# Optimization experiments

Measured on AMD Instinct MI355X. Metric: run time of the kernel, lower is better.

The kernel has to match this reference:

```python
import jax, jax.numpy as jnp
import numpy as np

TEMPERATURE = 0.5
EPS = 1e-12  # matches torch F.normalize default eps


def _l2_normalize(x):
    norm = jnp.sqrt(jnp.sum(x * x, axis=1, keepdims=True))
    return x / jnp.maximum(norm, EPS)


def setup_inputs() -> dict:
    key = jax.random.key(0)
    k1, k2 = jax.random.split(key)
    proj_1 = jax.random.normal(k1, (4096, 128), dtype=jnp.float32)
    proj_2 = jax.random.normal(k2, (4096, 128), dtype=jnp.float32)
    return {"proj_1": proj_1, "proj_2": proj_2}


def reference(proj_1, proj_2):
    batch_size = proj_1.shape[0]
    z_i = _l2_normalize(proj_1)
    z_j = _l2_normalize(proj_2)
    reps = jnp.concatenate([z_i, z_j], axis=0)  # [2B, D], rows unit-norm
    # cosine similarity of unit-norm rows == dot product -> single matmul
    sim = reps @ reps.T  # [2B, 2B]
    # positives: diag offset +B and -B
    pos_ij = jnp.diagonal(sim, offset=batch_size)   # [B]
    pos_ji = jnp.diagonal(sim, offset=-batch_size)  # [B]
    positives = jnp.concatenate([pos_ij, pos_ji], axis=0)  # [2B]
    nominator = jnp.exp(positives / TEMPERATURE)
    n = 2 * batch_size
    mask = 1.0 - jnp.eye(n, dtype=sim.dtype)
    denominator = jnp.sum(mask * jnp.exp(sim / TEMPERATURE), axis=1)  # [2B]
    all_losses = -jnp.log(nominator / denominator)
    return jnp.sum(all_losses) / n
```

## Files before the change

kernel.cpp:

```cpp
#include <hip/hip_runtime.h>
#include <stdint.h>


#define TEMP 0.5f
#define EXP2_SCALE 2.885390081777927f

typedef __bf16 bf16_t;
typedef bf16_t bf16x8 __attribute__((ext_vector_type(8)));
typedef float floatx4 __attribute__((ext_vector_type(4)));

typedef __attribute__((address_space(3))) uint32_t lds_u32;
typedef const __attribute__((address_space(1))) uint32_t glb_u32;

__device__ __forceinline__ unsigned short f32_to_bf16(float f) {
    union { float f; uint32_t u; } v; v.f = f;
    uint32_t u = v.u;
    uint32_t r = (u + 0x7FFFu + ((u >> 16) & 1u)) >> 16;
    return (unsigned short)r;
}

__device__ __forceinline__ bf16x8 as_bf16x8(uint4 v) {
    union { uint4 u; bf16x8 b; } c; c.u = v; return c.b;
}

__global__ __launch_bounds__(256) void norm_pos_kernel(
        const float* __restrict__ p1, const float* __restrict__ p2,
        unsigned short* __restrict__ reps, float* __restrict__ pos,
        float* __restrict__ rowsum, int B) {
    if (threadIdx.x < 8) {
        int z = blockIdx.x * 8 + threadIdx.x;
        if (z < 2 * B) rowsum[z] = 0.f;
    }

    int wave = threadIdx.x >> 6;
    int lane = threadIdx.x & 63;
    int i = blockIdx.x * 4 + wave;
    if (i >= B) return;

    const float2* r1 = (const float2*)(p1 + (size_t)i * 128);
    const float2* r2 = (const float2*)(p2 + (size_t)i * 128);
    float2 a = r1[lane];
    float2 b = r2[lane];
    float ss1 = a.x * a.x + a.y * a.y;
    float ss2 = b.x * b.x + b.y * b.y;
    float d   = a.x * b.x + a.y * b.y;
    #pragma unroll
    for (int off = 32; off > 0; off >>= 1) {
        ss1 += __shfl_xor(ss1, off);
        ss2 += __shfl_xor(ss2, off);
        d   += __shfl_xor(d,   off);
    }
    float rn1 = rsqrtf(fmaxf(ss1, 1e-24f));
    float rn2 = rsqrtf(fmaxf(ss2, 1e-24f));

    ushort2* z1 = (ushort2*)reps + (size_t)i * 64;
    ushort2* z2 = (ushort2*)reps + (size_t)(B + i) * 64;
    z1[lane] = make_ushort2(f32_to_bf16(a.x * rn1), f32_to_bf16(a.y * rn1));
    z2[lane] = make_ushort2(f32_to_bf16(b.x * rn2), f32_to_bf16(b.y * rn2));

    if (lane == 0) pos[i] = d * rn1 * rn2;
}

__global__ __launch_bounds__(256) void simexp_kernel(
        const unsigned short* __restrict__ reps,
        float* __restrict__ rowsum, int nt) {
    const int tid  = threadIdx.x;
    const int wave = tid >> 6;
    const int lane = tid & 63;
    const int quad = lane >> 4;
    const int l16  = lane & 15;

    int rem = (int)blockIdx.x;
    int by = 0;
    while (rem >= nt - by) { rem -= nt - by; ++by; }
    const int bx = by + rem;
    const bool diag = (bx == by);

    const int rowWave = by * 128 + wave * 32;
    const int colBase = bx * 128;

    const uint4* g = (const uint4*)reps;

    __shared__ __align__(16) unsigned short bbuf[2][2048];
    __shared__ float lds_cs[4][128];

    lds_cs[wave][lane]      = 0.f;
    lds_cs[wave][lane + 64] = 0.f;

    bf16x8 a[2][4];
    #pragma unroll
    for (int t = 0; t < 2; ++t)
        #pragma unroll
        for (int ks = 0; ks < 4; ++ks)
            a[t][ks] = as_bf16x8(g[(size_t)(rowWave + t * 16 + l16) * 16 + ks * 4 + quad]);

    float rs[2][4];
    #pragma unroll
    for (int t = 0; t < 2; ++t)
        #pragma unroll
        for (int r = 0; r < 4; ++r) rs[t][r] = 0.f;

    const int s_ks  = tid >> 6;
    const int s_fl  = tid & 63;
    const int s_fq  = s_fl >> 4;
    const int s_f16 = s_fl & 15;
    auto stage = [&](int buf, int ct) {
        const unsigned short* src = reps
            + (size_t)(colBase + ct * 16 + s_f16) * 128 + s_ks * 32 + s_fq * 8;
        __builtin_amdgcn_global_load_lds(
            (glb_u32*)src, (lds_u32*)&bbuf[buf][tid * 8], 16, 0, 0);
    };

    stage(0, 0);
    int cur = 0;

    #pragma unroll 1
    for (int ct = 0; ct < 8; ++ct) {
        __syncthreads();
        if (ct < 7) stage(cur ^ 1, ct + 1);

        bf16x8 b[4];
        #pragma unroll
        for (int ks = 0; ks < 4; ++ks)
            b[ks] = *(const bf16x8*)&bbuf[cur][ks * 512 + lane * 8];

        floatx4 acc[2];
        #pragma unroll
        for (int t = 0; t < 2; ++t) acc[t] = (floatx4){0.f, 0.f, 0.f, 0.f};
        #pragma unroll
        for (int ks = 0; ks < 4; ++ks)
            #pragma unroll
            for (int t = 0; t < 2; ++t)
                acc[t] = __builtin_amdgcn_mfma_f32_16x16x32_bf16(a[t][ks], b[ks], acc[t], 0, 0, 0);

        const int c = colBase + ct * 16 + l16;
        if (!diag) {
            float cs = 0.f;
            #pragma unroll
            for (int t = 0; t < 2; ++t)
                #pragma unroll
                for (int r = 0; r < 4; ++r) {
                    float e = exp2f(acc[t][r] * EXP2_SCALE);
                    rs[t][r] += e;
                    cs += e;
                }
            cs += __shfl_xor(cs, 16);
            cs += __shfl_xor(cs, 32);
            if (lane < 16) lds_cs[wave][ct * 16 + lane] += cs;
        } else {
            #pragma unroll
            for (int t = 0; t < 2; ++t) {
                const int rb = rowWave + t * 16 + quad * 4;
                #pragma unroll
                for (int r = 0; r < 4; ++r) {
                    float e = (rb + r == c) ? 0.f : exp2f(acc[t][r] * EXP2_SCALE);
                    rs[t][r] += e;
                }
            }
        }
        cur ^= 1;
    }

    #pragma unroll
    for (int off = 1; off < 16; off <<= 1)
        #pragma unroll
        for (int t = 0; t < 2; ++t)
            #pragma unroll
            for (int r = 0; r < 4; ++r)
                rs[t][r] += __shfl_xor(rs[t][r], off);

    if (l16 == 0) {
        #pragma unroll
        for (int t = 0; t < 2; ++t)
            #pragma unroll
            for (int r = 0; r < 4; ++r)
                atomicAdd(&rowsum[rowWave + t * 16 + quad * 4 + r], rs[t][r]);
    }

    if (!diag) {
        __syncthreads();
        if (tid < 128)
            atomicAdd(&rowsum[colBase + tid],
                      lds_cs[0][tid] + lds_cs[1][tid] + lds_cs[2][tid] + lds_cs[3][tid]);
    }
}

__global__ __launch_bounds__(1024) void finalize_kernel(
        const float* __restrict__ rowsum, const float* __restrict__ pos,
        float* __restrict__ out, int N2, int B) {
    float v = 0.f;
    const float4* r4 = (const float4*)rowsum;
    const int n4 = N2 >> 2;
    for (int k = threadIdx.x; k < n4; k += 1024) {
        float4 x = r4[k];
        v += logf(x.x) + logf(x.y) + logf(x.z) + logf(x.w);
    }
    float p = 0.f;
    const float4* p4 = (const float4*)pos;
    const int b4 = B >> 2;
    for (int i = threadIdx.x; i < b4; i += 1024) {
        float4 x = p4[i];
        p += x.x + x.y + x.z + x.w;
    }
    float local = v * (1.0f / (float)N2) - p * (1.0f / ((float)B * TEMP));

    #pragma unroll
    for (int off = 32; off > 0; off >>= 1) local += __shfl_xor(local, off);

    __shared__ float wsum[16];
    int wave = threadIdx.x >> 6, lane = threadIdx.x & 63;
    if (lane == 0) wsum[wave] = local;
    __syncthreads();
    if (threadIdx.x == 0) {
        float s = 0.f;
        for (int i = 0; i < 16; ++i) s += wsum[i];
        out[0] = s;
    }
}

extern "C" void kernel_launch(void* const* d_in, const int* in_sizes, int n_in,
                              void* d_out, int out_size, void* d_ws, size_t ws_size,
                              hipStream_t stream) {
    const float* p1 = (const float*)d_in[0];
    const float* p2 = (const float*)d_in[1];
    float* out = (float*)d_out;

    const int B  = in_sizes[0] / 128;
    const int N2 = 2 * B;

    unsigned short* reps = (unsigned short*)d_ws;
    float* rowsum = (float*)((char*)d_ws + (size_t)N2 * 256);
    float* pos    = rowsum + N2;

    norm_pos_kernel<<<dim3((B + 3) / 4), dim3(256), 0, stream>>>(p1, p2, reps, pos, rowsum, B);

    const int nt = N2 / 128;
    const int nb = nt * (nt + 1) / 2;
    simexp_kernel<<<dim3(nb), dim3(256), 0, stream>>>(reps, rowsum, nt);

    finalize_kernel<<<dim3(1), dim3(1024), 0, stream>>>(rowsum, pos, out, N2, B);
}
```

Baseline: 96.76 us.

## Preload full column tile into LDS upfront and widen norm kernel loads

The simexp kernel now issues all eight global-to-LDS column-tile loads at once into an 8-slot buffer, then synchronizes once, replacing the per-iteration double buffer and its repeated barriers. The goal is to take barriers and load latency out of the MFMA/exp loop. The cost is 32KB of LDS per block instead of 8KB, which may reduce occupancy. Separately, the normalization kernel has each half-wave handle one row with float4 loads and ushort4 stores, which halves the number of blocks and shortens the shuffle reduction.

```diff
diff --git a/kernel.cpp b/kernel.cpp
--- a/kernel.cpp
+++ b/kernel.cpp
@@ -27,25 +27,25 @@
         const float* __restrict__ p1, const float* __restrict__ p2,
         unsigned short* __restrict__ reps, float* __restrict__ pos,
         float* __restrict__ rowsum, int B) {
-    if (threadIdx.x < 8) {
-        int z = blockIdx.x * 8 + threadIdx.x;
+    if (threadIdx.x < 16) {
+        int z = blockIdx.x * 16 + threadIdx.x;
         if (z < 2 * B) rowsum[z] = 0.f;
     }
 
-    int wave = threadIdx.x >> 6;
-    int lane = threadIdx.x & 63;
-    int i = blockIdx.x * 4 + wave;
+    const int wave = threadIdx.x >> 6;
+    const int lane = threadIdx.x & 63;
+    const int half = lane >> 5;
+    const int h    = lane & 31;
+    const int i = blockIdx.x * 8 + wave * 2 + half;
     if (i >= B) return;
 
-    const float2* r1 = (const float2*)(p1 + (size_t)i * 128);
-    const float2* r2 = (const float2*)(p2 + (size_t)i * 128);
-    float2 a = r1[lane];
-    float2 b = r2[lane];
-    float ss1 = a.x * a.x + a.y * a.y;
-    float ss2 = b.x * b.x + b.y * b.y;
-    float d   = a.x * b.x + a.y * b.y;
-    #pragma unroll
-    for (int off = 32; off > 0; off >>= 1) {
+    float4 a = ((const float4*)(p1 + (size_t)i * 128))[h];
+    float4 b = ((const float4*)(p2 + (size_t)i * 128))[h];
+    float ss1 = a.x * a.x + a.y * a.y + a.z * a.z + a.w * a.w;
+    float ss2 = b.x * b.x + b.y * b.y + b.z * b.z + b.w * b.w;
+    float d   = a.x * b.x + a.y * b.y + a.z * b.z + a.w * b.w;
+    #pragma unroll
+    for (int off = 16; off > 0; off >>= 1) {
         ss1 += __shfl_xor(ss1, off);
         ss2 += __shfl_xor(ss2, off);
         d   += __shfl_xor(d,   off);
@@ -53,12 +53,14 @@
     float rn1 = rsqrtf(fmaxf(ss1, 1e-24f));
     float rn2 = rsqrtf(fmaxf(ss2, 1e-24f));
 
-    ushort2* z1 = (ushort2*)reps + (size_t)i * 64;
-    ushort2* z2 = (ushort2*)reps + (size_t)(B + i) * 64;
-    z1[lane] = make_ushort2(f32_to_bf16(a.x * rn1), f32_to_bf16(a.y * rn1));
-    z2[lane] = make_ushort2(f32_to_bf16(b.x * rn2), f32_to_bf16(b.y * rn2));
-
-    if (lane == 0) pos[i] = d * rn1 * rn2;
+    ((ushort4*)reps)[(size_t)i * 32 + h] = make_ushort4(
+        f32_to_bf16(a.x * rn1), f32_to_bf16(a.y * rn1),
+        f32_to_bf16(a.z * rn1), f32_to_bf16(a.w * rn1));
+    ((ushort4*)reps)[(size_t)(B + i) * 32 + h] = make_ushort4(
+        f32_to_bf16(b.x * rn2), f32_to_bf16(b.y * rn2),
+        f32_to_bf16(b.z * rn2), f32_to_bf16(b.w * rn2));
+
+    if (h == 0) pos[i] = d * rn1 * rn2;
 }
 
 __global__ __launch_bounds__(256) void simexp_kernel(
@@ -81,48 +83,45 @@
 
     const uint4* g = (const uint4*)reps;
 
-    __shared__ __align__(16) unsigned short bbuf[2][2048];
+    __shared__ __align__(16) unsigned short bbuf[8][2048];
     __shared__ float lds_cs[4][128];
 
     lds_cs[wave][lane]      = 0.f;
     lds_cs[wave][lane + 64] = 0.f;
-
-    bf16x8 a[2][4];
-    #pragma unroll
-    for (int t = 0; t < 2; ++t)
-        #pragma unroll
-        for (int ks = 0; ks < 4; ++ks)
-            a[t][ks] = as_bf16x8(g[(size_t)(rowWave + t * 16 + l16) * 16 + ks * 4 + quad]);
-
-    float rs[2][4];
-    #pragma unroll
-    for (int t = 0; t < 2; ++t)
-        #pragma unroll
-        for (int r = 0; r < 4; ++r) rs[t][r] = 0.f;
 
     const int s_ks  = tid >> 6;
     const int s_fl  = tid & 63;
     const int s_fq  = s_fl >> 4;
     const int s_f16 = s_fl & 15;
-    auto stage = [&](int buf, int ct) {
+    #pragma unroll
+    for (int ct = 0; ct < 8; ++ct) {
         const unsigned short* src = reps
             + (size_t)(colBase + ct * 16 + s_f16) * 128 + s_ks * 32 + s_fq * 8;
         __builtin_amdgcn_global_load_lds(
-            (glb_u32*)src, (lds_u32*)&bbuf[buf][tid * 8], 16, 0, 0);
-    };
-
-    stage(0, 0);
-    int cur = 0;
-
-    #pragma unroll 1
+            (glb_u32*)src, (lds_u32*)&bbuf[ct][tid * 8], 16, 0, 0);
+    }
+
+    bf16x8 a[2][4];
+    #pragma unroll
+    for (int t = 0; t < 2; ++t)
+        #pragma unroll
+        for (int ks = 0; ks < 4; ++ks)
+            a[t][ks] = as_bf16x8(g[(size_t)(rowWave + t * 16 + l16) * 16 + ks * 4 + quad]);
+
+    float rs[2][4];
+    #pragma unroll
+    for (int t = 0; t < 2; ++t)
+        #pragma unroll
+        for (int r = 0; r < 4; ++r) rs[t][r] = 0.f;
+
+    __syncthreads();
+
+    #pragma unroll 2
     for (int ct = 0; ct < 8; ++ct) {
-        __syncthreads();
-        if (ct < 7) stage(cur ^ 1, ct + 1);
-
         bf16x8 b[4];
         #pragma unroll
         for (int ks = 0; ks < 4; ++ks)
-            b[ks] = *(const bf16x8*)&bbuf[cur][ks * 512 + lane * 8];
+            b[ks] = *(const bf16x8*)&bbuf[ct][ks * 512 + lane * 8];
 
         floatx4 acc[2];
         #pragma unroll
@@ -158,7 +157,6 @@
                 }
             }
         }
-        cur ^= 1;
     }
 
     #pragma unroll
@@ -232,7 +230,7 @@
     float* rowsum = (float*)((char*)d_ws + (size_t)N2 * 256);
     float* pos    = rowsum + N2;
 
-    norm_pos_kernel<<<dim3((B + 3) / 4), dim3(256), 0, stream>>>(p1, p2, reps, pos, rowsum, B);
+    norm_pos_kernel<<<dim3((B + 7) / 8), dim3(256), 0, stream>>>(p1, p2, reps, pos, rowsum, B);
 
     const int nt = N2 / 128;
     const int nb = nt * (nt + 1) / 2;
```

Measured after the change: 91.51 us. 5.4% less time.
